# Kernel tuning notes

Hardware: AMD Instinct MI355X
Metric: run time of the kernel (lower is better)

The kernel has to match this reference:

```python
import jax, jax.numpy as jnp
import numpy as np

B, S, D, H = 4, 2048, 512, 8
DEPTH = D // H


def setup_inputs() -> dict:
    key = jax.random.key(0)
    ks = jax.random.split(key, 12)
    s = 0.02
    return {
        "q": jax.random.normal(ks[0], (B, S, D), jnp.float32),
        "k": jax.random.normal(ks[1], (B, S, D), jnp.float32),
        "v": jax.random.normal(ks[2], (B, S, D), jnp.float32),
        "mask": jax.random.randint(ks[3], (B, 1, 1, S), 0, 2, jnp.int32),
        "wq": jax.random.normal(ks[4], (D, D), jnp.float32) * s,
        "bq": jnp.zeros((D,), jnp.float32),
        "wk": jax.random.normal(ks[5], (D, D), jnp.float32) * s,
        "bk": jnp.zeros((D,), jnp.float32),
        "wv": jax.random.normal(ks[6], (D, D), jnp.float32) * s,
        "bv": jnp.zeros((D,), jnp.float32),
        "wo": jax.random.normal(ks[7], (D, D), jnp.float32) * s,
        "bo": jnp.zeros((D,), jnp.float32),
    }


def _split_heads(x):
    # [B,S,D] -> [B,H,S,depth]
    b = x.shape[0]
    return x.reshape(b, -1, H, DEPTH).transpose(0, 2, 1, 3)


def reference(q, k, v, mask, wq, bq, wk, bk, wv, bv, wo, bo):
    qh = _split_heads(q @ wq + bq)
    kh = _split_heads(k @ wk + bk)
    vh = _split_heads(v @ wv + bv)
    scale = 1.0 / jnp.sqrt(jnp.float32(DEPTH))
    logits = jnp.einsum("bhqd,bhkd->bhqk", qh, kh) * scale
    logits = logits + mask.astype(jnp.float32) * -1e9
    attn = jax.nn.softmax(logits, axis=-1)  # [B,H,Sq,Sk]
    out = jnp.einsum("bhqk,bhkd->bhqd", attn, vh)
    out = out.transpose(0, 2, 1, 3).reshape(q.shape[0], -1, D)
    out = out @ wo + bo
    return out, attn
```

## Files before the change

kernel.cpp:

```cpp
#include <hip/hip_runtime.h>

#define B_ 4
#define S_ 2048
#define D_ 512
#define H_ 8
#define DP_ 64
#define NT_ (S_/64)

typedef __attribute__((ext_vector_type(4))) float f32x4;
typedef __attribute__((ext_vector_type(8))) short short8;
typedef __attribute__((ext_vector_type(4))) int i32x4;

__device__ __forceinline__ short f2bf(float f){
  unsigned u = __float_as_uint(f);
  u += 0x7fff + ((u >> 16) & 1);
  return (short)(u >> 16);
}

__device__ __forceinline__ int cvtpk(float lo, float hi){
  int r;
  asm("v_cvt_pk_bf16_f32 %0, %1, %2" : "=v"(r) : "v"(lo), "v"(hi));
  return r;
}

#define SWZ(r, kb) ((r)*64 + ((kb) ^ (((r)&7)<<3)))
#define F2(r) ((((r)&3)) | ((((r)>>3)&1)<<2))
#define SWZ2(r, kb) ((r)*64 + ((kb) ^ (F2(r)<<3)))

#define WAITV(N) do{ asm volatile("s_waitcnt vmcnt(" #N ")" ::: "memory"); }while(0)
#define WAITLGKM() do{ asm volatile("s_waitcnt lgkmcnt(0)" ::: "memory"); }while(0)
#define BAR() do{ __builtin_amdgcn_s_barrier(); __builtin_amdgcn_sched_barrier(0); }while(0)

template<int NC>
__device__ __forceinline__ void stage_swz(const short* __restrict__ g, int rowStride,
                                          short* shbase, int w, int l){
  #pragma unroll
  for(int i = 0; i < NC; ++i){
    int byte = (w*NC + i)*1024 + l*16;
    int row = byte >> 7;
    int gs = ((byte >> 4) & 7) ^ (row & 7);
    const short* src = g + (size_t)row*rowStride + gs*8;
    __builtin_amdgcn_global_load_lds((const __attribute__((address_space(1))) void*)src,
        (__attribute__((address_space(3))) void*)(shbase + (w*NC + i)*512), 16, 0, 0);
  }
}
template<int NC>
__device__ __forceinline__ void stage_swz2(const short* __restrict__ g, int rowStride,
                                           short* shbase, int w, int l){
  #pragma unroll
  for(int i = 0; i < NC; ++i){
    int byte = (w*NC + i)*1024 + l*16;
    int row = byte >> 7;
    int gs = ((byte >> 4) & 7) ^ F2(row);
    const short* src = g + (size_t)row*rowStride + gs*8;
    __builtin_amdgcn_global_load_lds((const __attribute__((address_space(1))) void*)src,
        (__attribute__((address_space(3))) void*)(shbase + (w*NC + i)*512), 16, 0, 0);
  }
}

__global__ __launch_bounds__(256) void k_pre(const int* __restrict__ mask,
        const float* __restrict__ w0, const float* __restrict__ w1,
        const float* __restrict__ w2, const float* __restrict__ w3,
        short* __restrict__ wT, float* __restrict__ mb){
  __shared__ float tt[32][33];
  const int bi = blockIdx.x, t = threadIdx.x;
  if(bi < 1024){
    const int z = bi >> 8;
    const float* w = z == 0 ? w0 : z == 1 ? w1 : z == 2 ? w2 : w3;
    short* wt = wT + z * 262144;
    const int bxy = bi & 255;
    const int bx = (bxy & 15) * 32, by = (bxy >> 4) * 32;
    const int tx = t & 31, ty = t >> 5;
    #pragma unroll
    for(int i = 0; i < 32; i += 8) tt[ty + i][tx] = w[(by + ty + i) * D_ + bx + tx];
    __syncthreads();
    #pragma unroll
    for(int i = 0; i < 32; i += 8) wt[(bx + ty + i) * D_ + by + tx] = f2bf(tt[tx][ty + i]);
  } else {
    int i = (bi - 1024) * 256 + t;
    mb[i] = mask[i] ? -1.442695041e9f : 0.0f;
  }
}

__global__ __launch_bounds__(256) void k_gemm_qkv(const float* __restrict__ qf,
        const float* __restrict__ kf, const float* __restrict__ vf,
        const short* __restrict__ WTall, const float* __restrict__ b0,
        const float* __restrict__ b1, const float* __restrict__ b2,
        short* __restrict__ qh, short* __restrict__ kh, short* __restrict__ vvt){
  __shared__ __align__(16) short As[8192];
  __shared__ __align__(16) short Bs[8192];
  const int z = blockIdx.z;
  const float* X = z == 0 ? qf : (z == 1 ? kf : vf);
  const short* WT = WTall + (size_t)z * (D_*D_);
  const float* bias = z==0 ? b0 : (z==1 ? b1 : b2);
  const int t = threadIdx.x, l = t & 63, w = t >> 6;
  const int lr = l & 15, lg = l >> 4;
  const int m0 = blockIdx.x * 128, n0 = blockIdx.y * 128;
  const int wr = w >> 1, wc = w & 1;
  const float* Xb = X + (size_t)m0 * D_;
  const short* Wb = WT + (size_t)n0 * D_;
  f32x4 acc[4][4] = {};
  for(int kt = 0; kt < D_ / 64; ++kt){
    #pragma unroll
    for(int i = 0; i < 4; ++i){
      int e = t + 256 * i;
      int row = e >> 3, c8 = (e & 7) * 8;
      const float* src = Xb + (size_t)row * D_ + kt * 64 + c8;
      float4 f0 = *reinterpret_cast<const float4*>(src);
      float4 f1 = *reinterpret_cast<const float4*>(src + 4);
      i32x4 pk;
      pk[0] = cvtpk(f0.x, f0.y); pk[1] = cvtpk(f0.z, f0.w);
      pk[2] = cvtpk(f1.x, f1.y); pk[3] = cvtpk(f1.z, f1.w);
      *reinterpret_cast<i32x4*>(&As[SWZ(row, c8)]) = pk;
    }
    stage_swz<4>(Wb + kt*64, D_, Bs, w, l);
    __syncthreads();
    #pragma unroll
    for(int ks = 0; ks < 2; ++ks){
      const int kb = ks*32 + lg*8;
      short8 a[4], b[4];
      #pragma unroll
      for(int mt = 0; mt < 4; ++mt)
        a[mt] = *reinterpret_cast<const short8*>(&As[SWZ(wr*64 + mt*16 + lr, kb)]);
      #pragma unroll
      for(int nt = 0; nt < 4; ++nt)
        b[nt] = *reinterpret_cast<const short8*>(&Bs[SWZ(wc*64 + nt*16 + lr, kb)]);
      __builtin_amdgcn_s_setprio(1);
      #pragma unroll
      for(int mt = 0; mt < 4; ++mt)
        #pragma unroll
        for(int nt = 0; nt < 4; ++nt)
          acc[mt][nt] = __builtin_amdgcn_mfma_f32_16x16x32_bf16(a[mt], b[nt], acc[mt][nt], 0, 0, 0);
      __builtin_amdgcn_s_setprio(0);
    }
    __syncthreads();
  }
  #pragma unroll
  for(int mt = 0; mt < 4; ++mt){
    #pragma unroll
    for(int nt = 0; nt < 4; ++nt){
      const int n = n0 + wc*64 + nt*16 + lr;
      const int m4 = m0 + wr*64 + mt*16 + lg*4;
      float vals[4];
      #pragma unroll
      for(int r = 0; r < 4; ++r) vals[r] = acc[mt][nt][r] + bias[n];
      if(z == 2){
        short4 pv4;
        pv4.x = f2bf(vals[0]); pv4.y = f2bf(vals[1]); pv4.z = f2bf(vals[2]); pv4.w = f2bf(vals[3]);
        *reinterpret_cast<short4*>(&vvt[
            (((size_t)((m4 >> 11) * H_ + (n >> 6))) * DP_ + (n & 63)) * S_ + (m4 & 2047)]) = pv4;
      } else {
        short* dst = z == 0 ? qh : kh;
        #pragma unroll
        for(int r = 0; r < 4; ++r){
          int m = m4 + r;
          dst[(((size_t)((m >> 11) * H_ + (n >> 6))) * S_ + (m & 2047)) * DP_ + (n & 63)] = f2bf(vals[r]);
        }
      }
    }
  }
}

__global__ __launch_bounds__(256) void k_gemm_out(const short* __restrict__ X,
        const short* __restrict__ WT, const float* __restrict__ bias,
        float* __restrict__ Out){
  __shared__ __align__(16) short As[8192];
  __shared__ __align__(16) short Bs[8192];
  const int t = threadIdx.x, l = t & 63, w = t >> 6;
  const int lr = l & 15, lg = l >> 4;
  const int m0 = blockIdx.x * 128, n0 = blockIdx.y * 128;
  const int wr = w >> 1, wc = w & 1;
  const short* Xb = X + (size_t)m0 * D_;
  const short* Wb = WT + (size_t)n0 * D_;
  f32x4 acc[4][4] = {};
  for(int kt = 0; kt < D_ / 64; ++kt){
    stage_swz<4>(Xb + kt*64, D_, As, w, l);
    stage_swz<4>(Wb + kt*64, D_, Bs, w, l);
    __syncthreads();
    #pragma unroll
    for(int ks = 0; ks < 2; ++ks){
      const int kb = ks*32 + lg*8;
      short8 a[4], b[4];
      #pragma unroll
      for(int mt = 0; mt < 4; ++mt)
        a[mt] = *reinterpret_cast<const short8*>(&As[SWZ(wr*64 + mt*16 + lr, kb)]);
      #pragma unroll
      for(int nt = 0; nt < 4; ++nt)
        b[nt] = *reinterpret_cast<const short8*>(&Bs[SWZ(wc*64 + nt*16 + lr, kb)]);
      __builtin_amdgcn_s_setprio(1);
      #pragma unroll
      for(int mt = 0; mt < 4; ++mt)
        #pragma unroll
        for(int nt = 0; nt < 4; ++nt)
          acc[mt][nt] = __builtin_amdgcn_mfma_f32_16x16x32_bf16(a[mt], b[nt], acc[mt][nt], 0, 0, 0);
      __builtin_amdgcn_s_setprio(0);
    }
    __syncthreads();
  }
  #pragma unroll
  for(int mt = 0; mt < 4; ++mt){
    #pragma unroll
    for(int nt = 0; nt < 4; ++nt){
      const int n = n0 + wc*64 + nt*16 + lr;
      const int m4 = m0 + wr*64 + mt*16 + lg*4;
      #pragma unroll
      for(int r = 0; r < 4; ++r)
        Out[(size_t)(m4 + r) * D_ + n] = acc[mt][nt][r] + bias[n];
    }
  }
}

__global__ __launch_bounds__(512, 4) void k_attn(const short* __restrict__ qh,
                                                 const short* __restrict__ kh,
                                                 const short* __restrict__ vt,
                                                 const float* __restrict__ mb,
                                                 float* __restrict__ attn,
                                                 short* __restrict__ ctx){
  __shared__ __align__(16) short Sh[37376];
  const int t = threadIdx.x, l = t & 63, w = t >> 6;
  const int lr = l & 15, lg = l >> 4;
  const int wq = w & 3, g = w >> 2;
  int lin = blockIdx.y * 16 + blockIdx.x;
  int sw = (lin & 7) * 64 + (lin >> 3);
  const int bh = sw >> 4, b = bh >> 3, h = bh & 7;
  const int q0 = (sw & 15) * 128;
  const short* Qb = qh + (size_t)bh * S_ * DP_ + (size_t)q0 * DP_;
  const short* Kb = kh + (size_t)bh * S_ * DP_;
  const short* Vtb = vt + (size_t)bh * DP_ * S_;
  const float* Mbb = mb + b * S_;
  float* Mlds = (float*)Sh;
  short* KA = Sh + 4096;
  short* KB = Sh + 4096;
  short* VB = Sh + 20480;
  short* Qs = Sh + 28672;
  float* Ps_ = (float*)(Sh + 36864);
  const float scale2 = 0.125f * 1.442695041f;

  __builtin_amdgcn_global_load_lds(
      (const __attribute__((address_space(1))) void*)(Mbb + w*256 + l*4),
      (__attribute__((address_space(3))) void*)(Mlds + w*256 + l*4), 16, 0, 0);
  stage_swz2<2>(Qb, DP_, Qs, w, l);
  stage_swz2<1>(Kb,          DP_, KA,          w, l);
  stage_swz2<1>(Kb + 4096,   DP_, KA + 4096,   w, l);
  stage_swz2<1>(Kb + 2*4096, DP_, KA + 2*4096, w, l);
  stage_swz2<1>(Kb + 3*4096, DP_, KA + 3*4096, w, l);
  WAITV(4); BAR();
  short8 bq[2][2];
  #pragma unroll
  for(int qs = 0; qs < 2; ++qs){
    int r = wq * 32 + qs * 16 + lr;
    bq[qs][0] = *reinterpret_cast<const short8*>(&Qs[SWZ2(r, lg * 8)]);
    bq[qs][1] = *reinterpret_cast<const short8*>(&Qs[SWZ2(r, 32 + lg * 8)]);
  }
  const int grow = ((lr >> 2) << 3) + (lr & 3);

  float ps2[2] = {0.f, 0.f};
  for(int i = 0; i < NT_/2; ++i){
    if(i < NT_/2 - 1){ WAITV(2); } else { WAITV(0); }
    BAR();
    if(i + 2 < NT_/2){
      int tfa = 2*i + 4, tfb = 2*i + 5;
      stage_swz2<1>(Kb + (size_t)tfa * 4096, DP_, KA + (tfa % 6) * 4096, w, l);
      stage_swz2<1>(Kb + (size_t)tfb * 4096, DP_, KA + (tfb % 6) * 4096, w, l);
    }
    const int kt = 2*i + g;
    const short* Kc = KA + (kt % 6) * 4096;
    const float* Ml = Mlds + kt * 64;
    #pragma unroll
    for(int st = 0; st < 4; ++st){
      const int ks = st >> 1, h4 = st & 1;
      const int row = grow + h4 * 4 + ks * 32;
      const int mcol = ks * 32 + h4 * 4 + lg * 8;
      const float4 mv = *(const float4*)&Ml[mcol];
      short8 ak0 = *reinterpret_cast<const short8*>(&Kc[SWZ2(row, lg * 8)]);
      short8 ak1 = *reinterpret_cast<const short8*>(&Kc[SWZ2(row, 32 + lg * 8)]);
      __builtin_amdgcn_s_setprio(1);
      f32x4 c0 = {}, c1 = {};
      c0 = __builtin_amdgcn_mfma_f32_16x16x32_bf16(ak0, bq[0][0], c0, 0, 0, 0);
      c0 = __builtin_amdgcn_mfma_f32_16x16x32_bf16(ak1, bq[0][1], c0, 0, 0, 0);
      c1 = __builtin_amdgcn_mfma_f32_16x16x32_bf16(ak0, bq[1][0], c1, 0, 0, 0);
      c1 = __builtin_amdgcn_mfma_f32_16x16x32_bf16(ak1, bq[1][1], c1, 0, 0, 0);
      __builtin_amdgcn_s_setprio(0);
      ps2[0] += __builtin_amdgcn_exp2f(__builtin_fmaf(c0[0], scale2, mv.x));
      ps2[0] += __builtin_amdgcn_exp2f(__builtin_fmaf(c0[1], scale2, mv.y));
      ps2[0] += __builtin_amdgcn_exp2f(__builtin_fmaf(c0[2], scale2, mv.z));
      ps2[0] += __builtin_amdgcn_exp2f(__builtin_fmaf(c0[3], scale2, mv.w));
      ps2[1] += __builtin_amdgcn_exp2f(__builtin_fmaf(c1[0], scale2, mv.x));
      ps2[1] += __builtin_amdgcn_exp2f(__builtin_fmaf(c1[1], scale2, mv.y));
      ps2[1] += __builtin_amdgcn_exp2f(__builtin_fmaf(c1[2], scale2, mv.z));
      ps2[1] += __builtin_amdgcn_exp2f(__builtin_fmaf(c1[3], scale2, mv.w));
    }
  }
  #pragma unroll
  for(int qs = 0; qs < 2; ++qs){
    ps2[qs] += __shfl_xor(ps2[qs], 16, 64);
    ps2[qs] += __shfl_xor(ps2[qs], 32, 64);
  }
  Ps_[(w*2 + 0)*16 + lr] = ps2[0];
  Ps_[(w*2 + 1)*16 + lr] = ps2[1];
  WAITLGKM(); BAR();
  stage_swz2<1>(Kb,          DP_, KB,          w, l);
  stage_swz2<1>(Kb + 4096,   DP_, KB + 4096,   w, l);
  stage_swz2<1>(Vtb,         S_,  VB,          w, l);
  stage_swz2<1>(Vtb + 64,    S_,  VB + 4096,   w, l);
  stage_swz2<1>(Kb + 2*4096, DP_, KB + 2*4096, w, l);
  stage_swz2<1>(Kb + 3*4096, DP_, KB + 3*4096, w, l);
  stage_swz2<1>(Vtb + 2*64,  S_,  VB + 2*4096, w, l);
  stage_swz2<1>(Vtb + 3*64,  S_,  VB + 3*4096, w, l);
  const float rinv0 = 1.f / (ps2[0] + Ps_[((w^4)*2 + 0)*16 + lr]);
  const float rinv1 = 1.f / (ps2[1] + Ps_[((w^4)*2 + 1)*16 + lr]);

  f32x4 o[2][4] = {};
  for(int i = 0; i < NT_/2; ++i){
    if(i == 0){ WAITV(4); } else { WAITV(8); }
    BAR();
    if(i >= 1 && i + 1 < NT_/2){
      int tfa = 2*i + 2, tfb = 2*i + 3;
      stage_swz2<1>(Kb + (size_t)tfa * 4096, DP_, KB + (tfa & 3) * 4096, w, l);
      stage_swz2<1>(Kb + (size_t)tfb * 4096, DP_, KB + (tfb & 3) * 4096, w, l);
      stage_swz2<1>(Vtb + (size_t)tfa * 64,  S_,  VB + (tfa & 3) * 4096, w, l);
      stage_swz2<1>(Vtb + (size_t)tfb * 64,  S_,  VB + (tfb & 3) * 4096, w, l);
    }
    const int kt = 2*i + g;
    const short* Kc = KB + (kt & 3) * 4096;
    const short* Vc = VB + (kt & 3) * 4096;
    const float* Ml = Mlds + kt * 64;
    i32x4 pav[2][2];
    #pragma unroll
    for(int st = 0; st < 4; ++st){
      const int ks = st >> 1, h4 = st & 1;
      const int row = grow + h4 * 4 + ks * 32;
      const int mcol = ks * 32 + h4 * 4 + lg * 8;
      const float4 mv = *(const float4*)&Ml[mcol];
      short8 ak0 = *reinterpret_cast<const short8*>(&Kc[SWZ2(row, lg * 8)]);
      short8 ak1 = *reinterpret_cast<const short8*>(&Kc[SWZ2(row, 32 + lg * 8)]);
      __builtin_amdgcn_s_setprio(1);
      f32x4 c0 = {}, c1 = {};
      c0 = __builtin_amdgcn_mfma_f32_16x16x32_bf16(ak0, bq[0][0], c0, 0, 0, 0);
      c0 = __builtin_amdgcn_mfma_f32_16x16x32_bf16(ak1, bq[0][1], c0, 0, 0, 0);
      c1 = __builtin_amdgcn_mfma_f32_16x16x32_bf16(ak0, bq[1][0], c1, 0, 0, 0);
      c1 = __builtin_amdgcn_mfma_f32_16x16x32_bf16(ak1, bq[1][1], c1, 0, 0, 0);
      __builtin_amdgcn_s_setprio(0);
      float4 pw0, pw1;
      pw0.x = __builtin_amdgcn_exp2f(__builtin_fmaf(c0[0], scale2, mv.x)) * rinv0;
      pw0.y = __builtin_amdgcn_exp2f(__builtin_fmaf(c0[1], scale2, mv.y)) * rinv0;
      pw0.z = __builtin_amdgcn_exp2f(__builtin_fmaf(c0[2], scale2, mv.z)) * rinv0;
      pw0.w = __builtin_amdgcn_exp2f(__builtin_fmaf(c0[3], scale2, mv.w)) * rinv0;
      pw1.x = __builtin_amdgcn_exp2f(__builtin_fmaf(c1[0], scale2, mv.x)) * rinv1;
      pw1.y = __builtin_amdgcn_exp2f(__builtin_fmaf(c1[1], scale2, mv.y)) * rinv1;
      pw1.z = __builtin_amdgcn_exp2f(__builtin_fmaf(c1[2], scale2, mv.z)) * rinv1;
      pw1.w = __builtin_amdgcn_exp2f(__builtin_fmaf(c1[3], scale2, mv.w)) * rinv1;
      const int qr = q0 + wq * 32 + lr;
      *reinterpret_cast<float4*>(&attn[((size_t)bh * S_ + qr) * S_ + kt * 64 + mcol]) = pw0;
      *reinterpret_cast<float4*>(&attn[((size_t)bh * S_ + qr + 16) * S_ + kt * 64 + mcol]) = pw1;
      pav[0][ks][h4 * 2 + 0] = cvtpk(pw0.x, pw0.y);
      pav[0][ks][h4 * 2 + 1] = cvtpk(pw0.z, pw0.w);
      pav[1][ks][h4 * 2 + 0] = cvtpk(pw1.x, pw1.y);
      pav[1][ks][h4 * 2 + 1] = cvtpk(pw1.z, pw1.w);
    }
    #pragma unroll
    for(int ks = 0; ks < 2; ++ks){
      short8 pa0 = __builtin_bit_cast(short8, pav[0][ks]);
      short8 pa1 = __builtin_bit_cast(short8, pav[1][ks]);
      __builtin_amdgcn_s_setprio(1);
      #pragma unroll
      for(int dt = 0; dt < 4; ++dt){
        short8 vb = *reinterpret_cast<const short8*>(&Vc[SWZ2(dt * 16 + lr, ks * 32 + lg * 8)]);
        o[0][dt] = __builtin_amdgcn_mfma_f32_16x16x32_bf16(pa0, vb, o[0][dt], 0, 0, 0);
        o[1][dt] = __builtin_amdgcn_mfma_f32_16x16x32_bf16(pa1, vb, o[1][dt], 0, 0, 0);
      }
      __builtin_amdgcn_s_setprio(0);
    }
  }

  BAR();
  float* Oc = (float*)(Sh + 4096);
  if(g == 0){
    #pragma unroll
    for(int qs = 0; qs < 2; ++qs)
      #pragma unroll
      for(int dt = 0; dt < 4; ++dt)
        #pragma unroll
        for(int r = 0; r < 4; ++r)
          Oc[(wq*32 + qs*16 + lg*4 + r) * 65 + dt*16 + lr] = o[qs][dt][r];
  }
  WAITLGKM(); BAR();
  if(g == 1){
    #pragma unroll
    for(int qs = 0; qs < 2; ++qs){
      #pragma unroll
      for(int dt = 0; dt < 4; ++dt){
        #pragma unroll
        for(int r = 0; r < 4; ++r){
          float v = o[qs][dt][r] + Oc[(wq*32 + qs*16 + lg*4 + r) * 65 + dt*16 + lr];
          int qg = q0 + wq*32 + qs*16 + lg*4 + r;
          int dd = h * 64 + dt * 16 + lr;
          ctx[((size_t)b * S_ + qg) * D_ + dd] = f2bf(v);
        }
      }
    }
  }
}

extern "C" void kernel_launch(void* const* d_in, const int* in_sizes, int n_in,
                              void* d_out, int out_size, void* d_ws, size_t ws_size,
                              hipStream_t stream){
  const float* q  = (const float*)d_in[0];
  const float* k  = (const float*)d_in[1];
  const float* v  = (const float*)d_in[2];
  const int* mask = (const int*)d_in[3];
  const float* wq = (const float*)d_in[4];
  const float* bq = (const float*)d_in[5];
  const float* wk = (const float*)d_in[6];
  const float* bk = (const float*)d_in[7];
  const float* wv = (const float*)d_in[8];
  const float* bv = (const float*)d_in[9];
  const float* wo = (const float*)d_in[10];
  const float* bo = (const float*)d_in[11];

  float* out  = (float*)d_out;
  float* attn = out + (size_t)B_ * S_ * D_;

  char* ws = (char*)d_ws;
  short* qh  = (short*)(ws);
  short* kh  = (short*)(ws + 8388608);
  short* vvt = (short*)(ws + 16777216);
  short* ctx = (short*)(ws + 25165824);
  short* wT  = (short*)(ws + 33554432);
  float* mb  = (float*)(ws + 33554432 + 4 * 524288);

  hipLaunchKernelGGL(k_pre, dim3(1056), dim3(256), 0, stream,
                     mask, wq, wk, wv, wo, wT, mb);

  hipLaunchKernelGGL(k_gemm_qkv, dim3(64, 4, 3), dim3(256), 0, stream,
                     q, k, v, wT, bq, bk, bv, qh, kh, vvt);

  hipLaunchKernelGGL(k_attn, dim3(16, 32), dim3(512), 0, stream, qh, kh, vvt, mb, attn, ctx);

  hipLaunchKernelGGL(k_gemm_out, dim3(64, 4), dim3(256), 0, stream, ctx, wT + 3 * 262144, bo, out);
}
```

Baseline: 222.8 us.

## Read K, V, Q and mask directly from global memory instead of LDS staging

Removes the async global-to-LDS staging pipeline (swizzled multi-buffer K/V/Q/mask tiles with waitcnt and barriers) and has each wave load its MFMA operands straight from global memory, relying on the caches. LDS now holds only the row-sum exchange and the output reduction buffer. This cuts LDS footprint and barrier synchronisation, which may allow more occupancy. The cost is uncoalesced, latency-exposed global loads inside the MFMA loops with no prefetch, especially the strided V-transpose reads.

Measured after the change: 349.3 us. 56.8% more time.

```diff
diff --git a/kernel.cpp b/kernel.cpp
--- a/kernel.cpp
+++ b/kernel.cpp
@@ -24,12 +24,6 @@
 }
 
 #define SWZ(r, kb) ((r)*64 + ((kb) ^ (((r)&7)<<3)))
-#define F2(r) ((((r)&3)) | ((((r)>>3)&1)<<2))
-#define SWZ2(r, kb) ((r)*64 + ((kb) ^ (F2(r)<<3)))
-
-#define WAITV(N) do{ asm volatile("s_waitcnt vmcnt(" #N ")" ::: "memory"); }while(0)
-#define WAITLGKM() do{ asm volatile("s_waitcnt lgkmcnt(0)" ::: "memory"); }while(0)
-#define BAR() do{ __builtin_amdgcn_s_barrier(); __builtin_amdgcn_sched_barrier(0); }while(0)
 
 template<int NC>
 __device__ __forceinline__ void stage_swz(const short* __restrict__ g, int rowStride,
@@ -39,19 +33,6 @@
     int byte = (w*NC + i)*1024 + l*16;
     int row = byte >> 7;
     int gs = ((byte >> 4) & 7) ^ (row & 7);
-    const short* src = g + (size_t)row*rowStride + gs*8;
-    __builtin_amdgcn_global_load_lds((const __attribute__((address_space(1))) void*)src,
-        (__attribute__((address_space(3))) void*)(shbase + (w*NC + i)*512), 16, 0, 0);
-  }
-}
-template<int NC>
-__device__ __forceinline__ void stage_swz2(const short* __restrict__ g, int rowStride,
-                                           short* shbase, int w, int l){
-  #pragma unroll
-  for(int i = 0; i < NC; ++i){
-    int byte = (w*NC + i)*1024 + l*16;
-    int row = byte >> 7;
-    int gs = ((byte >> 4) & 7) ^ F2(row);
     const short* src = g + (size_t)row*rowStride + gs*8;
     __builtin_amdgcn_global_load_lds((const __attribute__((address_space(1))) void*)src,
         (__attribute__((address_space(3))) void*)(shbase + (w*NC + i)*512), 16, 0, 0);
@@ -216,7 +197,9 @@
                                                  const float* __restrict__ mb,
                                                  float* __restrict__ attn,
                                                  short* __restrict__ ctx){
-  __shared__ __align__(16) short Sh[37376];
+  __shared__ float ShF[8576];
+  float* Ps_ = ShF;
+  float* Oc  = ShF + 256;
   const int t = threadIdx.x, l = t & 63, w = t >> 6;
   const int lr = l & 15, lg = l >> 4;
   const int wq = w & 3, g = w >> 2;
@@ -228,52 +211,31 @@
   const short* Kb = kh + (size_t)bh * S_ * DP_;
   const short* Vtb = vt + (size_t)bh * DP_ * S_;
   const float* Mbb = mb + b * S_;
-  float* Mlds = (float*)Sh;
-  short* KA = Sh + 4096;
-  short* KB = Sh + 4096;
-  short* VB = Sh + 20480;
-  short* Qs = Sh + 28672;
-  float* Ps_ = (float*)(Sh + 36864);
   const float scale2 = 0.125f * 1.442695041f;
 
-  __builtin_amdgcn_global_load_lds(
-      (const __attribute__((address_space(1))) void*)(Mbb + w*256 + l*4),
-      (__attribute__((address_space(3))) void*)(Mlds + w*256 + l*4), 16, 0, 0);
-  stage_swz2<2>(Qb, DP_, Qs, w, l);
-  stage_swz2<1>(Kb,          DP_, KA,          w, l);
-  stage_swz2<1>(Kb + 4096,   DP_, KA + 4096,   w, l);
-  stage_swz2<1>(Kb + 2*4096, DP_, KA + 2*4096, w, l);
-  stage_swz2<1>(Kb + 3*4096, DP_, KA + 3*4096, w, l);
-  WAITV(4); BAR();
   short8 bq[2][2];
   #pragma unroll
   for(int qs = 0; qs < 2; ++qs){
-    int r = wq * 32 + qs * 16 + lr;
-    bq[qs][0] = *reinterpret_cast<const short8*>(&Qs[SWZ2(r, lg * 8)]);
-    bq[qs][1] = *reinterpret_cast<const short8*>(&Qs[SWZ2(r, 32 + lg * 8)]);
+    const short* qr = Qb + (size_t)(wq * 32 + qs * 16 + lr) * DP_;
+    bq[qs][0] = *reinterpret_cast<const short8*>(qr + lg * 8);
+    bq[qs][1] = *reinterpret_cast<const short8*>(qr + 32 + lg * 8);
   }
   const int grow = ((lr >> 2) << 3) + (lr & 3);
 
   float ps2[2] = {0.f, 0.f};
   for(int i = 0; i < NT_/2; ++i){
-    if(i < NT_/2 - 1){ WAITV(2); } else { WAITV(0); }
-    BAR();
-    if(i + 2 < NT_/2){
-      int tfa = 2*i + 4, tfb = 2*i + 5;
-      stage_swz2<1>(Kb + (size_t)tfa * 4096, DP_, KA + (tfa % 6) * 4096, w, l);
-      stage_swz2<1>(Kb + (size_t)tfb * 4096, DP_, KA + (tfb % 6) * 4096, w, l);
-    }
     const int kt = 2*i + g;
-    const short* Kc = KA + (kt % 6) * 4096;
-    const float* Ml = Mlds + kt * 64;
+    const short* Kt = Kb + (size_t)kt * 64 * DP_;
+    const float* Mt = Mbb + kt * 64;
     #pragma unroll
     for(int st = 0; st < 4; ++st){
       const int ks = st >> 1, h4 = st & 1;
       const int row = grow + h4 * 4 + ks * 32;
       const int mcol = ks * 32 + h4 * 4 + lg * 8;
-      const float4 mv = *(const float4*)&Ml[mcol];
-      short8 ak0 = *reinterpret_cast<const short8*>(&Kc[SWZ2(row, lg * 8)]);
-      short8 ak1 = *reinterpret_cast<const short8*>(&Kc[SWZ2(row, 32 + lg * 8)]);
+      const float4 mv = *reinterpret_cast<const float4*>(Mt + mcol);
+      const short* kr = Kt + (size_t)row * DP_;
+      short8 ak0 = *reinterpret_cast<const short8*>(kr + lg * 8);
+      short8 ak1 = *reinterpret_cast<const short8*>(kr + 32 + lg * 8);
       __builtin_amdgcn_s_setprio(1);
       f32x4 c0 = {}, c1 = {};
       c0 = __builtin_amdgcn_mfma_f32_16x16x32_bf16(ak0, bq[0][0], c0, 0, 0, 0);
@@ -298,42 +260,25 @@
   }
   Ps_[(w*2 + 0)*16 + lr] = ps2[0];
   Ps_[(w*2 + 1)*16 + lr] = ps2[1];
-  WAITLGKM(); BAR();
-  stage_swz2<1>(Kb,          DP_, KB,          w, l);
-  stage_swz2<1>(Kb + 4096,   DP_, KB + 4096,   w, l);
-  stage_swz2<1>(Vtb,         S_,  VB,          w, l);
-  stage_swz2<1>(Vtb + 64,    S_,  VB + 4096,   w, l);
-  stage_swz2<1>(Kb + 2*4096, DP_, KB + 2*4096, w, l);
-  stage_swz2<1>(Kb + 3*4096, DP_, KB + 3*4096, w, l);
-  stage_swz2<1>(Vtb + 2*64,  S_,  VB + 2*4096, w, l);
-  stage_swz2<1>(Vtb + 3*64,  S_,  VB + 3*4096, w, l);
+  __syncthreads();
   const float rinv0 = 1.f / (ps2[0] + Ps_[((w^4)*2 + 0)*16 + lr]);
   const float rinv1 = 1.f / (ps2[1] + Ps_[((w^4)*2 + 1)*16 + lr]);
 
   f32x4 o[2][4] = {};
   for(int i = 0; i < NT_/2; ++i){
-    if(i == 0){ WAITV(4); } else { WAITV(8); }
-    BAR();
-    if(i >= 1 && i + 1 < NT_/2){
-      int tfa = 2*i + 2, tfb = 2*i + 3;
-      stage_swz2<1>(Kb + (size_t)tfa * 4096, DP_, KB + (tfa & 3) * 4096, w, l);
-      stage_swz2<1>(Kb + (size_t)tfb * 4096, DP_, KB + (tfb & 3) * 4096, w, l);
-      stage_swz2<1>(Vtb + (size_t)tfa * 64,  S_,  VB + (tfa & 3) * 4096, w, l);
-      stage_swz2<1>(Vtb + (size_t)tfb * 64,  S_,  VB + (tfb & 3) * 4096, w, l);
-    }
     const int kt = 2*i + g;
-    const short* Kc = KB + (kt & 3) * 4096;
-    const short* Vc = VB + (kt & 3) * 4096;
-    const float* Ml = Mlds + kt * 64;
+    const short* Kt = Kb + (size_t)kt * 64 * DP_;
+    const float* Mt = Mbb + kt * 64;
     i32x4 pav[2][2];
     #pragma unroll
     for(int st = 0; st < 4; ++st){
       const int ks = st >> 1, h4 = st & 1;
       const int row = grow + h4 * 4 + ks * 32;
       const int mcol = ks * 32 + h4 * 4 + lg * 8;
-      const float4 mv = *(const float4*)&Ml[mcol];
-      short8 ak0 = *reinterpret_cast<const short8*>(&Kc[SWZ2(row, lg * 8)]);
-      short8 ak1 = *reinterpret_cast<const short8*>(&Kc[SWZ2(row, 32 + lg * 8)]);
+      const float4 mv = *reinterpret_cast<const float4*>(Mt + mcol);
+      const short* kr = Kt + (size_t)row * DP_;
+      short8 ak0 = *reinterpret_cast<const short8*>(kr + lg * 8);
+      short8 ak1 = *reinterpret_cast<const short8*>(kr + 32 + lg * 8);
       __builtin_amdgcn_s_setprio(1);
       f32x4 c0 = {}, c1 = {};
       c0 = __builtin_amdgcn_mfma_f32_16x16x32_bf16(ak0, bq[0][0], c0, 0, 0, 0);
@@ -362,19 +307,18 @@
     for(int ks = 0; ks < 2; ++ks){
       short8 pa0 = __builtin_bit_cast(short8, pav[0][ks]);
       short8 pa1 = __builtin_bit_cast(short8, pav[1][ks]);
-      __builtin_amdgcn_s_setprio(1);
       #pragma unroll
       for(int dt = 0; dt < 4; ++dt){
-        short8 vb = *reinterpret_cast<const short8*>(&Vc[SWZ2(dt * 16 + lr, ks * 32 + lg * 8)]);
+        short8 vb = *reinterpret_cast<const short8*>(
+            Vtb + (size_t)(dt * 16 + lr) * S_ + kt * 64 + ks * 32 + lg * 8);
+        __builtin_amdgcn_s_setprio(1);
         o[0][dt] = __builtin_amdgcn_mfma_f32_16x16x32_bf16(pa0, vb, o[0][dt], 0, 0, 0);
         o[1][dt] = __builtin_amdgcn_mfma_f32_16x16x32_bf16(pa1, vb, o[1][dt], 0, 0, 0);
+        __builtin_amdgcn_s_setprio(0);
       }
-      __builtin_amdgcn_s_setprio(0);
-    }
-  }
-
-  BAR();
-  float* Oc = (float*)(Sh + 4096);
+    }
+  }
+
   if(g == 0){
     #pragma unroll
     for(int qs = 0; qs < 2; ++qs)
@@ -384,7 +328,7 @@
         for(int r = 0; r < 4; ++r)
           Oc[(wq*32 + qs*16 + lg*4 + r) * 65 + dt*16 + lr] = o[qs][dt][r];
   }
-  WAITLGKM(); BAR();
+  __syncthreads();
   if(g == 1){
     #pragma unroll
     for(int qs = 0; qs < 2; ++qs){
```
